# Performance work log

Measured on AMD Instinct MI355X. Metric: run time of the kernel, lower is better.

Reference implementation:

```python
import jax, jax.numpy as jnp
import numpy as np

B, L, D = 32, 512, 128
H, D0, D2 = 8, 32, 32
SIGMA = 1.0
NEG = -10000.0


def setup_inputs() -> dict:
    key = jax.random.key(0)
    k_x, k_m, k1, k2, k3, k_w = jax.random.split(key, 6)
    X = jax.random.normal(k_x, (B, L, D), dtype=jnp.float32)
    # random padding mask; guarantee at least one valid item per row
    mask = jax.random.uniform(k_m, (B, L)) < 0.9
    mask = mask.at[:, 0].set(True)
    # nn.Linear(d, H*d0, bias=False): weight shape [H*d0, d], y = x @ W^T
    W1 = SIGMA * jax.random.normal(k1, (H * D0, D), dtype=jnp.float32)
    W2 = SIGMA * jax.random.normal(k2, (H * D0, D), dtype=jnp.float32)
    W3 = SIGMA * jax.random.normal(k3, (H * D2, D), dtype=jnp.float32)
    w = SIGMA * jax.random.normal(k_w, (H, D2), dtype=jnp.float32)
    return {"X": X, "mask": mask, "W1": W1, "W2": W2, "W3": W3, "w": w}


def reference(X, mask, W1, W2, W3, w):
    b, l, d = X.shape
    h, d2 = w.shape
    d0 = W1.shape[0] // h
    Q = (X @ W1.T).reshape(b, l, h, d0)
    K = (X @ W2.T).reshape(b, l, h, d0)
    V = (X @ W3.T).reshape(b, l, h, d2)
    # scores: [B, H, L, L]
    scores = jnp.einsum('blhd,bmhd->bhlm', Q, K) / jnp.sqrt(jnp.asarray(d0, X.dtype))
    # outer-product symmetric pad mask [B,1,L,L]
    am = (mask[:, None, None, :] & mask[:, None, :, None])
    scores = jnp.where(am, scores, jnp.asarray(NEG, X.dtype))
    attn = jax.nn.softmax(scores, axis=-1)
    out = jnp.einsum('bhlm,bmhd->blhd', attn, V)  # [B,L,H,D2]
    v = jnp.einsum('blhd,hd->bl', out, w) / jnp.sqrt(jnp.asarray(h, X.dtype))
    v = jnp.where(mask, v, jnp.asarray(NEG, X.dtype))
    probs = jax.nn.softmax(v, axis=-1)
    return probs
```

## Files before the change

kernel.cpp:

```cpp
#include <hip/hip_runtime.h>
#include <hip/hip_bf16.h>


typedef __attribute__((ext_vector_type(8))) short bf16x8;
typedef __attribute__((ext_vector_type(4))) float f32x4;
typedef __attribute__((ext_vector_type(8))) unsigned short ushort8;
typedef __attribute__((ext_vector_type(4))) unsigned short ushort4v;

#define NEG (-10000.0f)
#define LOG2E 1.4426950408889634f
#define QSCALE (0.17677669529663687f * LOG2E)

__device__ __forceinline__ unsigned short bf16_rn(float x, float* rep) {
  unsigned u = __float_as_uint(x);
  unsigned r = (u + 0x7FFFu + ((u >> 16) & 1u)) >> 16;
  *rep = __uint_as_float(r << 16);
  return (unsigned short)r;
}

__global__ __launch_bounds__(256) void convert_kernel(
    const float* __restrict__ X, const float* __restrict__ W1,
    const float* __restrict__ W2, const float* __restrict__ W3,
    const float* __restrict__ w,
    unsigned short* __restrict__ X2, unsigned short* __restrict__ Wc) {
  const int bx = blockIdx.x, t = threadIdx.x;
  if (bx < 1056) {
    const float* src;
    unsigned short* dst;
    int row, c;
    if (bx < 1024) {
      const size_t flat = (size_t)bx * 2048 + t * 8;
      row = (int)(flat >> 7); c = (int)(flat & 127);
      src = &X[flat];
      dst = &X2[(size_t)row * 256 + c];
    } else {
      const int flat = (bx - 1024) * 2048 + t * 8;
      row = flat >> 7; c = flat & 127;
      src = (row < 256) ? &W1[(size_t)row * 128 + c]
                        : &W2[(size_t)(row - 256) * 128 + c];
      dst = &Wc[(size_t)row * 256 + c];
    }
    float xv[8];
    *(float4*)&xv[0] = *(const float4*)src;
    *(float4*)&xv[4] = *(const float4*)(src + 4);
    ushort8 hi, lo;
#pragma unroll
    for (int i = 0; i < 8; ++i) {
      float hf, lf;
      hi[i] = bf16_rn(xv[i], &hf);
      lo[i] = bf16_rn(xv[i] - hf, &lf);
    }
    *(ushort8*)dst = hi;
    *(ushort8*)(dst + 128) = lo;
  } else {
    __shared__ float uS[8][128];
    if (t < 128) {
#pragma unroll
      for (int h = 0; h < 8; ++h) {
        float acc = 0.f;
#pragma unroll
        for (int d = 0; d < 32; ++d)
          acc += W3[(h * 32 + d) * 128 + t] * w[h * 32 + d];
        uS[h][t] = acc * 0.3535533905932738f;
      }
    }
    __syncthreads();
    {
      const int r = t >> 5, c = (t & 31) * 4;
      float4 v = *(float4*)&uS[r][c];
      float vv[4] = {v.x, v.y, v.z, v.w};
      ushort4v hi, lo;
#pragma unroll
      for (int i = 0; i < 4; ++i) {
        float hf, lf;
        hi[i] = bf16_rn(vv[i], &hf);
        lo[i] = bf16_rn(vv[i] - hf, &lf);
      }
      *(ushort4v*)&Wc[(size_t)(512 + r) * 256 + c] = hi;
      *(ushort4v*)&Wc[(size_t)(512 + r) * 256 + 128 + c] = lo;
    }
    const ushort8 z = {};
    for (int i = t; i < 1792; i += 256)
      *(ushort8*)&Wc[(size_t)520 * 256 + i * 8] = z;
  }
}

__global__ __launch_bounds__(256) void proj_kernel(
    const unsigned short* __restrict__ X2, const unsigned short* __restrict__ Wc,
    unsigned short* __restrict__ Q2, unsigned short* __restrict__ K2,
    float* __restrict__ Vw) {
  __shared__ unsigned short XS[64][72], WSd[64][72], WSx[64][72];
  const int t = threadIdx.x;
  const int row0 = blockIdx.x * 64, col0 = blockIdx.y * 64;
  const int w = t >> 6, lane = t & 63, g = lane >> 4, r16 = lane & 15;
  const int srow = t >> 2, su = (t & 3) * 16;

  f32x4 acc[4];
#pragma unroll
  for (int n = 0; n < 4; ++n) acc[n] = (f32x4){0.f, 0.f, 0.f, 0.f};

  for (int kc = 0; kc < 256; kc += 64) {
    const int kcx = (kc + 128) & 255;
    if (kc) __syncthreads();
    {
      const size_t xo = (size_t)(row0 + srow) * 256 + kc + su;
      const size_t wd = (size_t)(col0 + srow) * 256 + kc + su;
      const size_t wx = (size_t)(col0 + srow) * 256 + kcx + su;
      ushort8 a = *(const ushort8*)&X2[xo];
      ushort8 b = *(const ushort8*)&X2[xo + 8];
      ushort8 c = *(const ushort8*)&Wc[wd];
      ushort8 d = *(const ushort8*)&Wc[wd + 8];
      ushort8 e = *(const ushort8*)&Wc[wx];
      ushort8 f = *(const ushort8*)&Wc[wx + 8];
      *(ushort8*)&XS[srow][su] = a;
      *(ushort8*)&XS[srow][su + 8] = b;
      *(ushort8*)&WSd[srow][su] = c;
      *(ushort8*)&WSd[srow][su + 8] = d;
      *(ushort8*)&WSx[srow][su] = e;
      *(ushort8*)&WSx[srow][su + 8] = f;
    }
    __syncthreads();
#pragma unroll
    for (int ks = 0; ks < 2; ++ks) {
      bf16x8 ah = *(const bf16x8*)&XS[w * 16 + r16][ks * 32 + g * 8];
#pragma unroll
      for (int n = 0; n < 4; ++n) {
        bf16x8 bd = *(const bf16x8*)&WSd[n * 16 + r16][ks * 32 + g * 8];
        bf16x8 bx = *(const bf16x8*)&WSx[n * 16 + r16][ks * 32 + g * 8];
        acc[n] = __builtin_amdgcn_mfma_f32_16x16x32_bf16(ah, bd, acc[n], 0, 0, 0);
        acc[n] = __builtin_amdgcn_mfma_f32_16x16x32_bf16(ah, bx, acc[n], 0, 0, 0);
      }
    }
  }
#pragma unroll
  for (int n = 0; n < 4; ++n) {
    const int col = col0 + n * 16 + r16;
#pragma unroll
    for (int r = 0; r < 4; ++r) {
      const int row = row0 + w * 16 + g * 4 + r;
      const int b = row >> 9, l = row & 511;
      const float val = acc[n][r];
      if (col < 256) {
        const float sv = val * QSCALE;
        float hf, lf;
        const unsigned short hb = bf16_rn(sv, &hf);
        const unsigned short lb = bf16_rn(sv - hf, &lf);
        const size_t o = ((size_t)(b * 8 + (col >> 5)) * 512 + l) * 64 + (col & 31);
        Q2[o] = hb; Q2[o + 32] = lb;
      } else if (col < 512) {
        const int c2 = col - 256;
        float hf, lf;
        const unsigned short hb = bf16_rn(val, &hf);
        const unsigned short lb = bf16_rn(val - hf, &lf);
        const size_t o = ((size_t)(b * 8 + (c2 >> 5)) * 512 + l) * 64 + (c2 & 31);
        K2[o] = hb; K2[o + 32] = lb;
      } else if (col < 520) {
        Vw[(size_t)(b * 8 + (col - 512)) * 512 + l] = val;
      }
    }
  }
}

__global__ __launch_bounds__(512) void attn_kernel(
    const unsigned short* __restrict__ Q2, const unsigned short* __restrict__ K2,
    const float* __restrict__ Vw, const int* __restrict__ mask,
    float* __restrict__ vws) {
  __shared__ unsigned short KS[2][64][72];
  __shared__ float VwS[2][64], biasS[2][64];
  const int t = threadIdx.x;
  const int w = t >> 6, lane = t & 63, g = lane >> 4, r16 = lane & 15;
  const int qbase = blockIdx.x * 256, h = blockIdx.y, b = blockIdx.z;
  const size_t headoff = (size_t)(b * 8 + h) * 512;

  bf16x8 qf[2][2];
#pragma unroll
  for (int qt = 0; qt < 2; ++qt)
#pragma unroll
    for (int ks = 0; ks < 2; ++ks)
      qf[qt][ks] = *(const bf16x8*)
          &Q2[(headoff + qbase + w * 32 + qt * 16 + r16) * 64 + ks * 32 + g * 8];

  const int srow = t >> 3, su = (t & 7) * 8;
  ushort8 kreg = {};
  float vreg = 0.f, breg = 0.f;
  float m[2] = {-1e30f, -1e30f}, lsum[2] = {0.f, 0.f}, val[2] = {0.f, 0.f};

#define LOAD_CH(c)                                                        \
  {                                                                       \
    kreg = *(const ushort8*)&K2[(headoff + (c) * 64 + srow) * 64 + su];   \
    if (t < 64) vreg = Vw[headoff + (c) * 64 + t];                        \
    else if (t < 128)                                                     \
      breg = mask[b * 512 + (c) * 64 + (t - 64)] ? 0.f : NEG * LOG2E;     \
  }
#define WRITE_CH(c)                                                       \
  {                                                                       \
    const int bfi = (c) & 1;                                              \
    *(ushort8*)&KS[bfi][srow][su] = kreg;                                 \
    if (t < 64) VwS[bfi][t] = vreg;                                       \
    else if (t < 128) biasS[bfi][t - 64] = breg;                          \
  }

  LOAD_CH(0);
  WRITE_CH(0);
  __syncthreads();

  for (int c = 0; c < 8; ++c) {
    if (c < 7) LOAD_CH(c + 1);
    const int bfi = c & 1;
    bf16x8 a0[4], a1[4];
#pragma unroll
    for (int j = 0; j < 4; ++j) {
      a0[j] = *(const bf16x8*)&KS[bfi][j * 16 + r16][g * 8];
      a1[j] = *(const bf16x8*)&KS[bfi][j * 16 + r16][32 + g * 8];
    }
    f32x4 sc[4][2];
#pragma unroll
    for (int j = 0; j < 4; ++j)
#pragma unroll
      for (int qt = 0; qt < 2; ++qt) {
        f32x4 z = (f32x4){0.f, 0.f, 0.f, 0.f};
        z = __builtin_amdgcn_mfma_f32_16x16x32_bf16(a0[j], qf[qt][0], z, 0, 0, 0);
        z = __builtin_amdgcn_mfma_f32_16x16x32_bf16(a0[j], qf[qt][1], z, 0, 0, 0);
        z = __builtin_amdgcn_mfma_f32_16x16x32_bf16(a1[j], qf[qt][0], z, 0, 0, 0);
        sc[j][qt] = z;
      }
    float4 bs[4], vw4[4];
#pragma unroll
    for (int j = 0; j < 4; ++j) {
      bs[j]  = *(const float4*)&biasS[bfi][j * 16 + g * 4];
      vw4[j] = *(const float4*)&VwS[bfi][j * 16 + g * 4];
    }
#pragma unroll
    for (int qt = 0; qt < 2; ++qt) {
      float sb[4][4];
      float cmax = -1e30f;
#pragma unroll
      for (int j = 0; j < 4; ++j) {
        sb[j][0] = sc[j][qt][0] + bs[j].x;
        sb[j][1] = sc[j][qt][1] + bs[j].y;
        sb[j][2] = sc[j][qt][2] + bs[j].z;
        sb[j][3] = sc[j][qt][3] + bs[j].w;
#pragma unroll
        for (int r = 0; r < 4; ++r) cmax = fmaxf(cmax, sb[j][r]);
      }
      cmax = fmaxf(cmax, __shfl_xor(cmax, 16));
      cmax = fmaxf(cmax, __shfl_xor(cmax, 32));
      const float mnew = fmaxf(m[qt], cmax);
      const float f = __builtin_amdgcn_exp2f(m[qt] - mnew);
      m[qt] = mnew;
      float ls = lsum[qt] * f, vv = val[qt] * f;
#pragma unroll
      for (int j = 0; j < 4; ++j) {
        const float p0 = __builtin_amdgcn_exp2f(sb[j][0] - mnew);
        const float p1 = __builtin_amdgcn_exp2f(sb[j][1] - mnew);
        const float p2 = __builtin_amdgcn_exp2f(sb[j][2] - mnew);
        const float p3 = __builtin_amdgcn_exp2f(sb[j][3] - mnew);
        ls += (p0 + p1) + (p2 + p3);
        vv = fmaf(p0, vw4[j].x, vv);
        vv = fmaf(p1, vw4[j].y, vv);
        vv = fmaf(p2, vw4[j].z, vv);
        vv = fmaf(p3, vw4[j].w, vv);
      }
      lsum[qt] = ls; val[qt] = vv;
    }
    __syncthreads();
    if (c < 7) {
      WRITE_CH(c + 1);
      __syncthreads();
    }
  }
#pragma unroll
  for (int qt = 0; qt < 2; ++qt) {
    lsum[qt] += __shfl_xor(lsum[qt], 16);
    val[qt]  += __shfl_xor(val[qt], 16);
    lsum[qt] += __shfl_xor(lsum[qt], 32);
    val[qt]  += __shfl_xor(val[qt], 32);
  }
  if (lane < 16) {
#pragma unroll
    for (int qt = 0; qt < 2; ++qt)
      vws[headoff + qbase + w * 32 + qt * 16 + lane] = val[qt] / lsum[qt];
  }
#undef LOAD_CH
#undef WRITE_CH
}

__global__ __launch_bounds__(512) void final_kernel(
    const float* __restrict__ vws, const int* __restrict__ mask,
    float* __restrict__ out) {
  const int b = blockIdx.x, l = threadIdx.x;
  __shared__ float redm[8], reds[8];
  float v = 0.f;
#pragma unroll
  for (int h = 0; h < 8; ++h) v += vws[(size_t)(b * 8 + h) * 512 + l];
  if (mask[b * 512 + l] == 0) v = NEG;
  float mx = v;
#pragma unroll
  for (int off = 32; off >= 1; off >>= 1) mx = fmaxf(mx, __shfl_xor(mx, off));
  if ((l & 63) == 0) redm[l >> 6] = mx;
  __syncthreads();
  float M = redm[0];
#pragma unroll
  for (int i = 1; i < 8; ++i) M = fmaxf(M, redm[i]);
  const float e = __expf(v - M);
  float sm = e;
#pragma unroll
  for (int off = 32; off >= 1; off >>= 1) sm += __shfl_xor(sm, off);
  if ((l & 63) == 0) reds[l >> 6] = sm;
  __syncthreads();
  float S = 0.f;
#pragma unroll
  for (int i = 0; i < 8; ++i) S += reds[i];
  out[b * 512 + l] = e / S;
}

extern "C" void kernel_launch(void* const* d_in, const int* in_sizes, int n_in,
                              void* d_out, int out_size, void* d_ws, size_t ws_size,
                              hipStream_t stream) {
  const float* X  = (const float*)d_in[0];
  const int*  mk  = (const int*)d_in[1];
  const float* W1 = (const float*)d_in[2];
  const float* W2 = (const float*)d_in[3];
  const float* W3 = (const float*)d_in[4];
  const float* w  = (const float*)d_in[5];
  float* out = (float*)d_out;

  char* ws = (char*)d_ws;
  unsigned short* X2 = (unsigned short*)ws;
  unsigned short* Wc = X2 + (size_t)16384 * 256;
  unsigned short* Q2 = Wc + (size_t)576 * 256;
  unsigned short* K2 = Q2 + (size_t)32 * 8 * 512 * 64;
  float* Vw  = (float*)(K2 + (size_t)32 * 8 * 512 * 64);
  float* vws = Vw + (size_t)32 * 8 * 512;

  convert_kernel<<<dim3(1057), dim3(256), 0, stream>>>(X, W1, W2, W3, w, X2, Wc);
  proj_kernel<<<dim3(256, 9), dim3(256), 0, stream>>>(X2, Wc, Q2, K2, Vw);
  attn_kernel<<<dim3(2, 8, 32), dim3(512), 0, stream>>>(Q2, K2, Vw, mk, vws);
  final_kernel<<<dim3(32), dim3(512), 0, stream>>>(vws, mk, out);
}
```

Baseline: 60.25 us.

## Load full K head into LDS once; per-lane online softmax, merge at end

```diff
diff --git a/kernel.cpp b/kernel.cpp
--- a/kernel.cpp
+++ b/kernel.cpp
@@ -161,17 +161,25 @@
   }
 }
 
-__global__ __launch_bounds__(512) void attn_kernel(
+__global__ __launch_bounds__(512, 4) void attn_kernel(
     const unsigned short* __restrict__ Q2, const unsigned short* __restrict__ K2,
     const float* __restrict__ Vw, const int* __restrict__ mask,
     float* __restrict__ vws) {
-  __shared__ unsigned short KS[2][64][72];
-  __shared__ float VwS[2][64], biasS[2][64];
+  __shared__ unsigned short KS[512][72];
+  __shared__ float VwS[512], biasS[512];
   const int t = threadIdx.x;
   const int w = t >> 6, lane = t & 63, g = lane >> 4, r16 = lane & 15;
   const int qbase = blockIdx.x * 256, h = blockIdx.y, b = blockIdx.z;
   const size_t headoff = (size_t)(b * 8 + h) * 512;
 
+#pragma unroll
+  for (int i = 0; i < 8; ++i) {
+    const int flat = i * 512 + t, row = flat >> 3, cg = (flat & 7) * 8;
+    *(ushort8*)&KS[row][cg] = *(const ushort8*)&K2[(headoff + row) * 64 + cg];
+  }
+  VwS[t] = Vw[headoff + t];
+  biasS[t] = mask[b * 512 + t] ? 0.f : NEG * LOG2E;
+
   bf16x8 qf[2][2];
 #pragma unroll
   for (int qt = 0; qt < 2; ++qt)
@@ -180,109 +188,78 @@
       qf[qt][ks] = *(const bf16x8*)
           &Q2[(headoff + qbase + w * 32 + qt * 16 + r16) * 64 + ks * 32 + g * 8];
 
-  const int srow = t >> 3, su = (t & 7) * 8;
-  ushort8 kreg = {};
-  float vreg = 0.f, breg = 0.f;
-  float m[2] = {-1e30f, -1e30f}, lsum[2] = {0.f, 0.f}, val[2] = {0.f, 0.f};
-
-#define LOAD_CH(c)                                                        \
-  {                                                                       \
-    kreg = *(const ushort8*)&K2[(headoff + (c) * 64 + srow) * 64 + su];   \
-    if (t < 64) vreg = Vw[headoff + (c) * 64 + t];                        \
-    else if (t < 128)                                                     \
-      breg = mask[b * 512 + (c) * 64 + (t - 64)] ? 0.f : NEG * LOG2E;     \
-  }
-#define WRITE_CH(c)                                                       \
-  {                                                                       \
-    const int bfi = (c) & 1;                                              \
-    *(ushort8*)&KS[bfi][srow][su] = kreg;                                 \
-    if (t < 64) VwS[bfi][t] = vreg;                                       \
-    else if (t < 128) biasS[bfi][t - 64] = breg;                          \
-  }
-
-  LOAD_CH(0);
-  WRITE_CH(0);
   __syncthreads();
 
+  float m[2] = {-3e38f, -3e38f}, ls[2] = {0.f, 0.f}, vv[2] = {0.f, 0.f};
+
   for (int c = 0; c < 8; ++c) {
-    if (c < 7) LOAD_CH(c + 1);
-    const int bfi = c & 1;
     bf16x8 a0[4], a1[4];
 #pragma unroll
     for (int j = 0; j < 4; ++j) {
-      a0[j] = *(const bf16x8*)&KS[bfi][j * 16 + r16][g * 8];
-      a1[j] = *(const bf16x8*)&KS[bfi][j * 16 + r16][32 + g * 8];
-    }
-    f32x4 sc[4][2];
-#pragma unroll
-    for (int j = 0; j < 4; ++j)
-#pragma unroll
-      for (int qt = 0; qt < 2; ++qt) {
-        f32x4 z = (f32x4){0.f, 0.f, 0.f, 0.f};
+      a0[j] = *(const bf16x8*)&KS[c * 64 + j * 16 + r16][g * 8];
+      a1[j] = *(const bf16x8*)&KS[c * 64 + j * 16 + r16][32 + g * 8];
+    }
+    float4 bs4[4], vw4[4];
+#pragma unroll
+    for (int j = 0; j < 4; ++j) {
+      bs4[j] = *(const float4*)&biasS[c * 64 + j * 16 + g * 4];
+      vw4[j] = *(const float4*)&VwS[c * 64 + j * 16 + g * 4];
+    }
+#pragma unroll
+    for (int qt = 0; qt < 2; ++qt) {
+      f32x4 sc[4];
+#pragma unroll
+      for (int j = 0; j < 4; ++j) {
+        f32x4 z = (f32x4){bs4[j].x, bs4[j].y, bs4[j].z, bs4[j].w};
         z = __builtin_amdgcn_mfma_f32_16x16x32_bf16(a0[j], qf[qt][0], z, 0, 0, 0);
         z = __builtin_amdgcn_mfma_f32_16x16x32_bf16(a0[j], qf[qt][1], z, 0, 0, 0);
         z = __builtin_amdgcn_mfma_f32_16x16x32_bf16(a1[j], qf[qt][0], z, 0, 0, 0);
-        sc[j][qt] = z;
-      }
-    float4 bs[4], vw4[4];
-#pragma unroll
-    for (int j = 0; j < 4; ++j) {
-      bs[j]  = *(const float4*)&biasS[bfi][j * 16 + g * 4];
-      vw4[j] = *(const float4*)&VwS[bfi][j * 16 + g * 4];
-    }
-#pragma unroll
-    for (int qt = 0; qt < 2; ++qt) {
-      float sb[4][4];
-      float cmax = -1e30f;
-#pragma unroll
-      for (int j = 0; j < 4; ++j) {
-        sb[j][0] = sc[j][qt][0] + bs[j].x;
-        sb[j][1] = sc[j][qt][1] + bs[j].y;
-        sb[j][2] = sc[j][qt][2] + bs[j].z;
-        sb[j][3] = sc[j][qt][3] + bs[j].w;
-#pragma unroll
-        for (int r = 0; r < 4; ++r) cmax = fmaxf(cmax, sb[j][r]);
-      }
-      cmax = fmaxf(cmax, __shfl_xor(cmax, 16));
-      cmax = fmaxf(cmax, __shfl_xor(cmax, 32));
+        sc[j] = z;
+      }
+      float cm01 = fmaxf(fmaxf(sc[0][0], sc[0][1]), fmaxf(sc[0][2], sc[0][3]));
+      float cm23 = fmaxf(fmaxf(sc[1][0], sc[1][1]), fmaxf(sc[1][2], sc[1][3]));
+      float cm45 = fmaxf(fmaxf(sc[2][0], sc[2][1]), fmaxf(sc[2][2], sc[2][3]));
+      float cm67 = fmaxf(fmaxf(sc[3][0], sc[3][1]), fmaxf(sc[3][2], sc[3][3]));
+      const float cmax = fmaxf(fmaxf(cm01, cm23), fmaxf(cm45, cm67));
       const float mnew = fmaxf(m[qt], cmax);
       const float f = __builtin_amdgcn_exp2f(m[qt] - mnew);
       m[qt] = mnew;
-      float ls = lsum[qt] * f, vv = val[qt] * f;
+      float l = ls[qt] * f, v = vv[qt] * f;
 #pragma unroll
       for (int j = 0; j < 4; ++j) {
-        const float p0 = __builtin_amdgcn_exp2f(sb[j][0] - mnew);
-        const float p1 = __builtin_amdgcn_exp2f(sb[j][1] - mnew);
-        const float p2 = __builtin_amdgcn_exp2f(sb[j][2] - mnew);
-        const float p3 = __builtin_amdgcn_exp2f(sb[j][3] - mnew);
-        ls += (p0 + p1) + (p2 + p3);
-        vv = fmaf(p0, vw4[j].x, vv);
-        vv = fmaf(p1, vw4[j].y, vv);
-        vv = fmaf(p2, vw4[j].z, vv);
-        vv = fmaf(p3, vw4[j].w, vv);
-      }
-      lsum[qt] = ls; val[qt] = vv;
-    }
-    __syncthreads();
-    if (c < 7) {
-      WRITE_CH(c + 1);
-      __syncthreads();
+        const float p0 = __builtin_amdgcn_exp2f(sc[j][0] - mnew);
+        const float p1 = __builtin_amdgcn_exp2f(sc[j][1] - mnew);
+        const float p2 = __builtin_amdgcn_exp2f(sc[j][2] - mnew);
+        const float p3 = __builtin_amdgcn_exp2f(sc[j][3] - mnew);
+        l += (p0 + p1) + (p2 + p3);
+        v = fmaf(p0, vw4[j].x, v);
+        v = fmaf(p1, vw4[j].y, v);
+        v = fmaf(p2, vw4[j].z, v);
+        v = fmaf(p3, vw4[j].w, v);
+      }
+      ls[qt] = l; vv[qt] = v;
     }
   }
 #pragma unroll
   for (int qt = 0; qt < 2; ++qt) {
-    lsum[qt] += __shfl_xor(lsum[qt], 16);
-    val[qt]  += __shfl_xor(val[qt], 16);
-    lsum[qt] += __shfl_xor(lsum[qt], 32);
-    val[qt]  += __shfl_xor(val[qt], 32);
+#pragma unroll
+    for (int off = 16; off <= 32; off <<= 1) {
+      const float mo = __shfl_xor(m[qt], off);
+      const float lo_ = __shfl_xor(ls[qt], off);
+      const float vo = __shfl_xor(vv[qt], off);
+      const float m2 = fmaxf(m[qt], mo);
+      const float fa = __builtin_amdgcn_exp2f(m[qt] - m2);
+      const float fb = __builtin_amdgcn_exp2f(mo - m2);
+      ls[qt] = ls[qt] * fa + lo_ * fb;
+      vv[qt] = vv[qt] * fa + vo * fb;
+      m[qt] = m2;
+    }
   }
   if (lane < 16) {
 #pragma unroll
     for (int qt = 0; qt < 2; ++qt)
-      vws[headoff + qbase + w * 32 + qt * 16 + lane] = val[qt] / lsum[qt];
-  }
-#undef LOAD_CH
-#undef WRITE_CH
+      vws[headoff + qbase + w * 32 + qt * 16 + lane] = vv[qt] / ls[qt];
+  }
 }
 
 __global__ __launch_bounds__(512) void final_kernel(
```

Result: slower. 63.02 us (+4.6%).
